# Kernel optimization log

Measured on AMD Instinct MI355X. Metric: run time of the kernel, lower is better.

The kernel has to match this reference:

```python
import jax, jax.numpy as jnp
import numpy as np

N_EMBD = 768

def setup_inputs() -> dict:
    key = jax.random.key(0)
    k1, k2, k3, k4 = jax.random.split(key, 4)
    B, T, head_size = 16, 1024, 128
    x = jax.random.normal(k1, (B, T, N_EMBD), dtype=jnp.float32)
    # nn.Linear(in, out, bias=False): weight stored as (out, in); we store transposed (in, out)
    s = 1.0 / np.sqrt(N_EMBD)
    Wk = jax.random.uniform(k2, (N_EMBD, head_size), jnp.float32, -s, s)
    Wq = jax.random.uniform(k3, (N_EMBD, head_size), jnp.float32, -s, s)
    Wv = jax.random.uniform(k4, (N_EMBD, head_size), jnp.float32, -s, s)
    return {"x": x, "Wk": Wk, "Wq": Wq, "Wv": Wv}

def reference(x, Wk, Wq, Wv):
    B, T, C = x.shape  # C == n_embd == 768
    k = jnp.einsum('btc,ch->bth', x, Wk)
    q = jnp.einsum('btc,ch->bth', x, Wq)
    v = jnp.einsum('btc,ch->bth', x, Wv)
    # NOTE: original scales by C**-0.5 with C = n_embd (768), not head_size.
    wei = jnp.einsum('bth,bsh->bts', q, k) * (C ** -0.5)  # (B, T, T)
    causal = jnp.tril(jnp.ones((T, T), dtype=bool))
    wei = jnp.where(causal, wei, -jnp.inf)
    wei = jax.nn.softmax(wei, axis=-1)
    # dropout p=0.0 -> identity
    return jnp.einsum('bts,bsh->bth', wei, v)
```

## Files before the change

### kernel.cpp

```cpp
#include <hip/hip_runtime.h>
#include <math.h>

#define NTOK   16384
#define NEMBD  768
#define HDIM   128

typedef __attribute__((ext_vector_type(8)))  short short8;
typedef __attribute__((ext_vector_type(16))) float floatx16;

#define MFMA32(a,b,c) __builtin_amdgcn_mfma_f32_32x32x16_bf16(a,b,c,0,0,0)

__device__ __forceinline__ unsigned short f2bf(float f) {
    unsigned u = __float_as_uint(f);
    u += 0x7fff + ((u >> 16) & 1);
    return (unsigned short)(u >> 16);
}
__device__ __forceinline__ unsigned pack2(float a, float b) {
    return (unsigned)f2bf(a) | ((unsigned)f2bf(b) << 16);
}
__device__ __forceinline__ unsigned pack2_trunc(float a, float b) {
    return __builtin_amdgcn_perm(__float_as_uint(b), __float_as_uint(a),
                                 0x07060302u);
}
__device__ __forceinline__ void gl_lds16(const void* gptr, void* lptr) {
    __builtin_amdgcn_global_load_lds(
        (const __attribute__((address_space(1))) unsigned int*)gptr,
        (__attribute__((address_space(3))) unsigned int*)lptr, 16, 0, 0);
}

__global__ __launch_bounds__(256) void prep_w(
    const float* __restrict__ Wk, const float* __restrict__ Wq,
    const float* __restrict__ Wv, unsigned short* __restrict__ wt)
{
    __shared__ float T[128 * 65];

    const int tid = threadIdx.x;
    const int bw = blockIdx.x / 12;
    const int ct = blockIdx.x % 12;
    const int c0 = ct * 64;
    const float* W = (bw == 0) ? Wk : ((bw == 1) ? Wq : Wv);
    const float scale = (bw == 1)
        ? (0.03608439182435161f * 1.4426950408889634f) : 1.0f;

    #pragma unroll
    for (int pass = 0; pass < 8; ++pass) {
        int idx = pass * 256 + tid;
        int c  = idx >> 5;
        int d4 = idx & 31;
        float4 v = ((const float4*)W)[(size_t)(c0 + c) * 32 + d4];
        v.x *= scale; v.y *= scale; v.z *= scale; v.w *= scale;
        T[(d4 * 4 + 0) * 65 + c] = v.x;
        T[(d4 * 4 + 1) * 65 + c] = v.y;
        T[(d4 * 4 + 2) * 65 + c] = v.z;
        T[(d4 * 4 + 3) * 65 + c] = v.w;
    }
    __syncthreads();

    #pragma unroll
    for (int pass = 0; pass < 4; ++pass) {
        int idx = pass * 256 + tid;
        int d  = idx >> 3;
        int c8 = idx & 7;
        const float* row = &T[d * 65 + c8 * 8];
        uint4 u = make_uint4(pack2(row[0], row[1]), pack2(row[2], row[3]),
                             pack2(row[4], row[5]), pack2(row[6], row[7]));
        *(uint4*)&wt[(size_t)bw * (HDIM * NEMBD) + d * NEMBD + c0 + c8 * 8] = u;
    }
}

__global__ __launch_bounds__(256) void qkv_fused(
    const float* __restrict__ x, const unsigned short* __restrict__ wt,
    unsigned short* __restrict__ kb, unsigned short* __restrict__ qb,
    unsigned short* __restrict__ vT)
{
    __shared__ __align__(16) char As[4096];
    __shared__ __align__(16) char Bs[49152];

    const int tid = threadIdx.x, w = tid >> 6, lane = tid & 63;
    const int l31 = lane & 31, h = lane >> 5;
    const int r8 = lane >> 3, c8 = lane & 7;
    const int m0 = blockIdx.x * 32;
    const int arow = tid >> 3, ac = tid & 7;

    floatx16 acc[3];
    #pragma unroll
    for (int j = 0; j < 3; ++j)
        #pragma unroll
        for (int i = 0; i < 16; ++i) acc[j][i] = 0.f;

    const float* asrc = x + (size_t)(m0 + arow) * NEMBD + ac * 8;
    float4 a0 = ((const float4*)asrc)[0];
    float4 a1 = ((const float4*)asrc)[1];

    for (int it = 0; it < 12; ++it) {
        const int k0 = it * 64;
        __syncthreads();
        #pragma unroll
        for (int j = 0; j < 12; ++j) {
            int rowb = w * 96 + j * 8;
            int row  = rowb + r8;
            gl_lds16((const char*)wt + ((size_t)row * NEMBD + k0) * 2
                         + ((c8 ^ (row & 7)) * 16),
                     Bs + rowb * 128);
        }
        {
            uint4 u = make_uint4(pack2(a0.x, a0.y), pack2(a0.z, a0.w),
                                 pack2(a1.x, a1.y), pack2(a1.z, a1.w));
            *(uint4*)(As + arow * 128 + ((ac ^ (arow & 7)) * 16)) = u;
        }
        if (it < 11) {
            const float4* src = (const float4*)(asrc + (it + 1) * 64);
            a0 = src[0];
            a1 = src[1];
        }
        __syncthreads();
        #pragma unroll
        for (int ks = 0; ks < 4; ++ks) {
            short8 af = *(const short8*)(As + l31 * 128
                                         + (((2*ks + h) ^ (l31 & 7)) * 16));
            #pragma unroll
            for (int j = 0; j < 3; ++j) {
                int br = w * 96 + j * 32 + l31;
                short8 bf = *(const short8*)(Bs + br * 128
                                             + (((2*ks + h) ^ (br & 7)) * 16));
                acc[j] = MFMA32(af, bf, acc[j]);
            }
        }
    }

    #pragma unroll
    for (int j = 0; j < 3; ++j) {
        int n0 = w * 96 + j * 32;
        if (n0 < 256) {
            unsigned short* outp = (n0 < 128) ? kb : qb;
            int d = (n0 & 127) + l31;
            #pragma unroll
            for (int r = 0; r < 16; ++r) {
                int t = m0 + (r & 3) + 8 * (r >> 2) + 4 * h;
                outp[(size_t)t * HDIM + d] = f2bf(acc[j][r]);
            }
        } else {
            int d = (n0 - 256) + l31, b = m0 >> 10, tloc = m0 & 1023;
            #pragma unroll
            for (int g = 0; g < 4; ++g) {
                int t = tloc + 8 * g + 4 * h;
                uint2 u = make_uint2(pack2(acc[j][4*g+0], acc[j][4*g+1]),
                                     pack2(acc[j][4*g+2], acc[j][4*g+3]));
                *(uint2*)((char*)vT + (((size_t)(b * HDIM + d)) * 1024 + t) * 2) = u;
            }
        }
    }
}

__global__ __launch_bounds__(256) void attn_mfma(
    const unsigned short* __restrict__ qb, const unsigned short* __restrict__ kb,
    const unsigned short* __restrict__ vT, float* __restrict__ out)
{
    __shared__ __align__(16) float Obuf[4 * 32 * 128];
    __shared__ float lred[128];

    const int tid = threadIdx.x, w = tid >> 6, lane = tid & 63;
    const int l31 = lane & 31, h = lane >> 5;
    const int u  = blockIdx.x & 255;
    const int b  = u & 15, p = u >> 4;
    const int qt = (blockIdx.x >> 8) ? (31 - p) : p;

    const char* kb_b = (const char*)kb + (size_t)b * (1024 * 256);
    const char* qb_b = (const char*)qb + (size_t)b * (1024 * 256);
    const char* vT_b = (const char*)vT + (size_t)b * (HDIM * 2048);

    short8 qf[8];
    {
        const char* qrow = qb_b + (size_t)(qt * 32 + l31) * 256 + h * 16;
        #pragma unroll
        for (int ks = 0; ks < 8; ++ks)
            qf[ks] = *(const short8*)(qrow + ks * 32);
    }

    floatx16 o[4];
    #pragma unroll
    for (int nt = 0; nt < 4; ++nt)
        #pragma unroll
        for (int i = 0; i < 16; ++i) o[nt][i] = 0.f;
    float l_r = 0.f;

    short8 kf[8];
    if (w <= qt) {
        const char* krow = kb_b + (size_t)(w * 32 + l31) * 256 + h * 16;
        #pragma unroll
        for (int ks = 0; ks < 8; ++ks)
            kf[ks] = *(const short8*)(krow + ks * 32);
    }

    for (int st = w; st <= qt; st += 4) {
        short8 vf[8];
        {
            const char* vrow0 = vT_b + (size_t)l31 * 2048 + (size_t)st * 64 + h * 16;
            #pragma unroll
            for (int nt = 0; nt < 4; ++nt) {
                const char* vr = vrow0 + (size_t)nt * (32 * 2048);
                vf[nt * 2 + 0] = *(const short8*)(vr + 0);
                vf[nt * 2 + 1] = *(const short8*)(vr + 32);
            }
        }
        floatx16 s;
        #pragma unroll
        for (int i = 0; i < 16; ++i) s[i] = 0.f;
        #pragma unroll
        for (int ks = 0; ks < 8; ++ks) s = MFMA32(kf[ks], qf[ks], s);

        if (st + 4 <= qt) {
            const char* krow = kb_b + (size_t)((st + 4) * 32 + l31) * 256 + h * 16;
            #pragma unroll
            for (int ks = 0; ks < 8; ++ks)
                kf[ks] = *(const short8*)(krow + ks * 32);
        }

        if (st == qt) {
            #pragma unroll
            for (int r = 0; r < 16; ++r) {
                int key = (r & 3) + 8 * (r >> 2) + 4 * h;
                if (key > l31) s[r] = -1e30f;
            }
        }
        float p16[16], psum = 0.f;
        #pragma unroll
        for (int r = 0; r < 16; ++r) {
            p16[r] = __builtin_amdgcn_exp2f(s[r]);
            psum += p16[r];
        }
        l_r += psum;

        unsigned own[8], rcv[8];
        #pragma unroll
        for (int i = 0; i < 8; ++i) own[i] = pack2_trunc(p16[2*i], p16[2*i+1]);
        #pragma unroll
        for (int i = 0; i < 8; ++i) rcv[i] = (unsigned)__shfl_xor((int)own[i], 32, 64);
        short8 pf[2];
        {
            union { short8 v; unsigned uu[4]; } f0, f1;
            if (h == 0) {
                f0.uu[0]=own[0]; f0.uu[1]=own[1]; f0.uu[2]=rcv[0]; f0.uu[3]=rcv[1];
                f1.uu[0]=own[4]; f1.uu[1]=own[5]; f1.uu[2]=rcv[4]; f1.uu[3]=rcv[5];
            } else {
                f0.uu[0]=rcv[2]; f0.uu[1]=rcv[3]; f0.uu[2]=own[2]; f0.uu[3]=own[3];
                f1.uu[0]=rcv[6]; f1.uu[1]=rcv[7]; f1.uu[2]=own[6]; f1.uu[3]=own[7];
            }
            pf[0] = f0.v; pf[1] = f1.v;
        }
        #pragma unroll
        for (int nt = 0; nt < 4; ++nt) {
            o[nt] = MFMA32(vf[nt * 2 + 0], pf[0], o[nt]);
            o[nt] = MFMA32(vf[nt * 2 + 1], pf[1], o[nt]);
        }
    }

    l_r += __shfl_xor(l_r, 32, 64);
    if (lane < 32) lred[w * 32 + l31] = l_r;
    {
        float* mybuf = &Obuf[w * 4096];
        #pragma unroll
        for (int nt = 0; nt < 4; ++nt) {
            #pragma unroll
            for (int g = 0; g < 4; ++g) {
                int chunk = nt * 8 + 2 * g + h;
                int slot  = (chunk & 24) | ((chunk & 7) ^ (l31 & 7));
                *((float4*)&mybuf[l31 * 128] + slot) =
                    make_float4(o[nt][4*g+0], o[nt][4*g+1],
                                o[nt][4*g+2], o[nt][4*g+3]);
            }
        }
    }
    __syncthreads();
    {
        int q  = tid >> 3;
        int cb = (tid & 7) * 4;
        float inv = 1.f / (lred[q] + lred[32 + q] + lred[64 + q] + lred[96 + q]);
        #pragma unroll
        for (int cc = 0; cc < 4; ++cc) {
            int chunk = cb + cc;
            int slot  = (chunk & 24) | ((chunk & 7) ^ (q & 7));
            float4 v0 = *((float4*)&Obuf[0 * 4096 + q * 128] + slot);
            float4 v1 = *((float4*)&Obuf[1 * 4096 + q * 128] + slot);
            float4 v2 = *((float4*)&Obuf[2 * 4096 + q * 128] + slot);
            float4 v3 = *((float4*)&Obuf[3 * 4096 + q * 128] + slot);
            float4 v = make_float4((v0.x + v1.x + v2.x + v3.x) * inv,
                                   (v0.y + v1.y + v2.y + v3.y) * inv,
                                   (v0.z + v1.z + v2.z + v3.z) * inv,
                                   (v0.w + v1.w + v2.w + v3.w) * inv);
            *(float4*)&out[((size_t)(b * 1024 + qt * 32 + q)) * HDIM + chunk * 4] = v;
        }
    }
}

extern "C" void kernel_launch(void* const* d_in, const int* in_sizes, int n_in,
                              void* d_out, int out_size, void* d_ws, size_t ws_size,
                              hipStream_t stream)
{
    const float* x  = (const float*)d_in[0];
    const float* Wk = (const float*)d_in[1];
    const float* Wq = (const float*)d_in[2];
    const float* Wv = (const float*)d_in[3];
    float* outp = (float*)d_out;

    char* ws = (char*)d_ws;
    unsigned short* wt = (unsigned short*)(ws);
    unsigned short* kb = (unsigned short*)(ws + 589824);
    unsigned short* qb = (unsigned short*)(ws + 4784128);
    unsigned short* vT = (unsigned short*)(ws + 8978432);

    prep_w<<<36, 256, 0, stream>>>(Wk, Wq, Wv, wt);
    qkv_fused<<<512, 256, 0, stream>>>(x, wt, kb, qb, vT);
    attn_mfma<<<512, 256, 0, stream>>>(qb, kb, vT, outp);
}
```

Baseline: 129.8 us.

## Retile QKV projection to 64x192 block tiles with 2x2 wave layout

```diff
diff --git a/kernel.cpp b/kernel.cpp
--- a/kernel.cpp
+++ b/kernel.cpp
@@ -32,22 +32,23 @@
     const float* __restrict__ Wk, const float* __restrict__ Wq,
     const float* __restrict__ Wv, unsigned short* __restrict__ wt)
 {
-    __shared__ float T[128 * 65];
+    __shared__ float T[64 * 65];
 
     const int tid = threadIdx.x;
-    const int bw = blockIdx.x / 12;
-    const int ct = blockIdx.x % 12;
-    const int c0 = ct * 64;
+    const int bw  = blockIdx.x / 24;
+    const int rem = blockIdx.x % 24;
+    const int ct  = rem >> 1, dh = rem & 1;
+    const int c0  = ct * 64, d0 = dh * 64;
     const float* W = (bw == 0) ? Wk : ((bw == 1) ? Wq : Wv);
     const float scale = (bw == 1)
         ? (0.03608439182435161f * 1.4426950408889634f) : 1.0f;
 
     #pragma unroll
-    for (int pass = 0; pass < 8; ++pass) {
+    for (int pass = 0; pass < 4; ++pass) {
         int idx = pass * 256 + tid;
-        int c  = idx >> 5;
-        int d4 = idx & 31;
-        float4 v = ((const float4*)W)[(size_t)(c0 + c) * 32 + d4];
+        int c  = idx >> 4;
+        int d4 = idx & 15;
+        float4 v = ((const float4*)W)[(size_t)(c0 + c) * 32 + dh * 16 + d4];
         v.x *= scale; v.y *= scale; v.z *= scale; v.w *= scale;
         T[(d4 * 4 + 0) * 65 + c] = v.x;
         T[(d4 * 4 + 1) * 65 + c] = v.y;
@@ -57,14 +58,15 @@
     __syncthreads();
 
     #pragma unroll
-    for (int pass = 0; pass < 4; ++pass) {
+    for (int pass = 0; pass < 2; ++pass) {
         int idx = pass * 256 + tid;
         int d  = idx >> 3;
         int c8 = idx & 7;
         const float* row = &T[d * 65 + c8 * 8];
         uint4 u = make_uint4(pack2(row[0], row[1]), pack2(row[2], row[3]),
                              pack2(row[4], row[5]), pack2(row[6], row[7]));
-        *(uint4*)&wt[(size_t)bw * (HDIM * NEMBD) + d * NEMBD + c0 + c8 * 8] = u;
+        *(uint4*)&wt[(size_t)bw * (HDIM * NEMBD) + (size_t)(d0 + d) * NEMBD
+                     + c0 + c8 * 8] = u;
     }
 }
 
@@ -73,14 +75,17 @@
     unsigned short* __restrict__ kb, unsigned short* __restrict__ qb,
     unsigned short* __restrict__ vT)
 {
-    __shared__ __align__(16) char As[4096];
-    __shared__ __align__(16) char Bs[49152];
+    __shared__ __align__(16) char As[8192];
+    __shared__ __align__(16) char Bs[24576];
 
     const int tid = threadIdx.x, w = tid >> 6, lane = tid & 63;
     const int l31 = lane & 31, h = lane >> 5;
     const int r8 = lane >> 3, c8 = lane & 7;
-    const int m0 = blockIdx.x * 32;
-    const int arow = tid >> 3, ac = tid & 7;
+    const int wm = w >> 1, wn = w & 1;
+    const int mtile = blockIdx.x >> 1, nh = blockIdx.x & 1;
+    const int m0 = mtile * 64;
+    const int nbase = nh * 192;
+    const int arow = tid >> 2, ac = tid & 3;
 
     floatx16 acc[3];
     #pragma unroll
@@ -88,39 +93,45 @@
         #pragma unroll
         for (int i = 0; i < 16; ++i) acc[j][i] = 0.f;
 
-    const float* asrc = x + (size_t)(m0 + arow) * NEMBD + ac * 8;
+    const float* asrc = x + (size_t)(m0 + arow) * NEMBD + ac * 16;
     float4 a0 = ((const float4*)asrc)[0];
     float4 a1 = ((const float4*)asrc)[1];
+    float4 a2 = ((const float4*)asrc)[2];
+    float4 a3 = ((const float4*)asrc)[3];
 
     for (int it = 0; it < 12; ++it) {
         const int k0 = it * 64;
         __syncthreads();
         #pragma unroll
-        for (int j = 0; j < 12; ++j) {
-            int rowb = w * 96 + j * 8;
+        for (int j = 0; j < 6; ++j) {
+            int rowb = w * 48 + j * 8;
             int row  = rowb + r8;
-            gl_lds16((const char*)wt + ((size_t)row * NEMBD + k0) * 2
+            gl_lds16((const char*)wt + ((size_t)(nbase + row) * NEMBD + k0) * 2
                          + ((c8 ^ (row & 7)) * 16),
                      Bs + rowb * 128);
         }
         {
-            uint4 u = make_uint4(pack2(a0.x, a0.y), pack2(a0.z, a0.w),
-                                 pack2(a1.x, a1.y), pack2(a1.z, a1.w));
-            *(uint4*)(As + arow * 128 + ((ac ^ (arow & 7)) * 16)) = u;
+            uint4 u0 = make_uint4(pack2(a0.x, a0.y), pack2(a0.z, a0.w),
+                                  pack2(a1.x, a1.y), pack2(a1.z, a1.w));
+            uint4 u1 = make_uint4(pack2(a2.x, a2.y), pack2(a2.z, a2.w),
+                                  pack2(a3.x, a3.y), pack2(a3.z, a3.w));
+            int cA = 2 * ac, cB = 2 * ac + 1;
+            *(uint4*)(As + arow * 128 + ((cA ^ (arow & 7)) * 16)) = u0;
+            *(uint4*)(As + arow * 128 + ((cB ^ (arow & 7)) * 16)) = u1;
         }
         if (it < 11) {
             const float4* src = (const float4*)(asrc + (it + 1) * 64);
-            a0 = src[0];
-            a1 = src[1];
+            a0 = src[0]; a1 = src[1]; a2 = src[2]; a3 = src[3];
         }
         __syncthreads();
         #pragma unroll
         for (int ks = 0; ks < 4; ++ks) {
-            short8 af = *(const short8*)(As + l31 * 128
-                                         + (((2*ks + h) ^ (l31 & 7)) * 16));
+            int ar = wm * 32 + l31;
+            short8 af = *(const short8*)(As + ar * 128
+                                         + (((2*ks + h) ^ (ar & 7)) * 16));
             #pragma unroll
             for (int j = 0; j < 3; ++j) {
-                int br = w * 96 + j * 32 + l31;
+                int br = wn * 96 + j * 32 + l31;
                 short8 bf = *(const short8*)(Bs + br * 128
                                              + (((2*ks + h) ^ (br & 7)) * 16));
                 acc[j] = MFMA32(af, bf, acc[j]);
@@ -128,19 +139,20 @@
         }
     }
 
+    const int tbase = m0 + wm * 32;
     #pragma unroll
     for (int j = 0; j < 3; ++j) {
-        int n0 = w * 96 + j * 32;
+        int n0 = nbase + wn * 96 + j * 32;
         if (n0 < 256) {
             unsigned short* outp = (n0 < 128) ? kb : qb;
             int d = (n0 & 127) + l31;
             #pragma unroll
             for (int r = 0; r < 16; ++r) {
-                int t = m0 + (r & 3) + 8 * (r >> 2) + 4 * h;
+                int t = tbase + (r & 3) + 8 * (r >> 2) + 4 * h;
                 outp[(size_t)t * HDIM + d] = f2bf(acc[j][r]);
             }
         } else {
-            int d = (n0 - 256) + l31, b = m0 >> 10, tloc = m0 & 1023;
+            int d = (n0 - 256) + l31, b = m0 >> 10, tloc = (m0 & 1023) + wm * 32;
             #pragma unroll
             for (int g = 0; g < 4; ++g) {
                 int t = tloc + 8 * g + 4 * h;
@@ -309,7 +321,7 @@
     unsigned short* qb = (unsigned short*)(ws + 4784128);
     unsigned short* vT = (unsigned short*)(ws + 8978432);
 
-    prep_w<<<36, 256, 0, stream>>>(Wk, Wq, Wv, wt);
+    prep_w<<<72, 256, 0, stream>>>(Wk, Wq, Wv, wt);
     qkv_fused<<<512, 256, 0, stream>>>(x, wt, kb, qb, vT);
     attn_mfma<<<512, 256, 0, stream>>>(qb, kb, vT, outp);
 }
```

Result: faster. 127.1 us (-2.1%).
